# Performance work log

Measured on AMD Instinct MI355X. Metric: run time of the kernel, lower is better.

Reference implementation:

```python
import jax, jax.numpy as jnp
import numpy as np

N = 4096
IN_DIM = 512
NHEADS = 12
HEAD_DIM = 64


def setup_inputs() -> dict:
    key = jax.random.key(0)
    k_g, k_adj, k_wk, k_wq, k_hw = jax.random.split(key, 5)
    g = jax.random.normal(k_g, (N, IN_DIM), dtype=jnp.float32)
    # binary adjacency, broadcastable over the head axis of the [q,k,h] scores
    adj = jax.random.randint(k_adj, (N, N, 1), 0, 2).astype(jnp.float32)
    Wk = 0.002 * jax.random.normal(k_wk, (NHEADS, HEAD_DIM, IN_DIM), dtype=jnp.float32)
    Wq = 0.002 * jax.random.normal(k_wq, (NHEADS, HEAD_DIM, IN_DIM), dtype=jnp.float32)
    Hw = 0.002 * jax.random.normal(k_hw, (NHEADS, NHEADS), dtype=jnp.float32)
    Bk = jnp.zeros((NHEADS, HEAD_DIM), dtype=jnp.float32)
    Bq = jnp.zeros((NHEADS, HEAD_DIM), dtype=jnp.float32)
    betas = jnp.ones((NHEADS,), dtype=jnp.float32) / np.sqrt(HEAD_DIM).astype(np.float32)
    return {"g": g, "adj": adj, "Wk": Wk, "Wq": Wq, "Hw": Hw, "Bk": Bk, "Bq": Bq, "betas": betas}


def reference(g, adj, Wk, Wq, Hw, Bk, Bq, betas):
    def energy(g_):
        K = jnp.einsum('kd,hzd->khz', g_, Wk) + Bk          # [N, h, z]
        Q = jnp.einsum('qd,hzd->qhz', g_, Wq) + Bq          # [N, h, z]
        A1 = jnp.einsum('h,qhz,khz->hqk', betas, Q, K)      # [h, q, k]
        A11 = (jnp.transpose(A1, (1, 2, 0)) @ Hw) * adj      # [q, k, h], adjacency-gated
        A11 = jnp.where(A11 == 0, -jnp.inf, A11)
        A21 = jax.nn.logsumexp(A11, axis=1)                  # [q, h]
        A21 = jnp.where(A21 == -jnp.inf, 0.0, A21)
        A31 = A21.sum(0)                                     # [h]
        return ((-1.0 / betas) * A31).sum()
    # the module's __call__ returns (energy, dE/dg)
    return jax.value_and_grad(energy)(g)
```

## Files before the change

kernel.cpp:

```cpp
#include <hip/hip_runtime.h>
#include <stdint.h>

#define N_TOK 4096
#define DIM_IN 512
#define NH 12
#define HD 64
#define CDIM 768

using f32x4  = __attribute__((ext_vector_type(4))) float;
using f32x16 = __attribute__((ext_vector_type(16))) float;
using bf16x8 = __attribute__((ext_vector_type(8))) short;

static __device__ __forceinline__ unsigned short f2bf(float f){
    union { float f; unsigned int u; } v; v.f = f;
    unsigned int r = v.u + 0x7fffu + ((v.u >> 16) & 1u);
    return (unsigned short)(r >> 16);
}

__global__ __launch_bounds__(256) void proj_kernel(
    const float* __restrict__ g, const float* __restrict__ W,
    const float* __restrict__ B, const float* __restrict__ scale,
    unsigned short* __restrict__ out)
{
    __shared__ float at[16][68];
    __shared__ float bt[16][68];
    const int n0 = blockIdx.x * 64, c0 = blockIdx.y * 64;
    const int t  = threadIdx.x;
    const int tx = t & 15, ty = t >> 4;
    const int lr = t >> 2, lk = (t & 3) * 4;
    float acc[4][4] = {};
    f32x4 pg = *(const f32x4*)&g[(size_t)(n0 + lr) * DIM_IN + lk];
    f32x4 pw = *(const f32x4*)&W[(size_t)(c0 + lr) * DIM_IN + lk];
    for (int d0 = 0; d0 < DIM_IN; d0 += 16){
        __syncthreads();
        at[lk+0][lr] = pg[0]; at[lk+1][lr] = pg[1]; at[lk+2][lr] = pg[2]; at[lk+3][lr] = pg[3];
        bt[lk+0][lr] = pw[0]; bt[lk+1][lr] = pw[1]; bt[lk+2][lr] = pw[2]; bt[lk+3][lr] = pw[3];
        __syncthreads();
        {
            const int dn = (d0 + 16 < DIM_IN) ? d0 + 16 : 0;
            pg = *(const f32x4*)&g[(size_t)(n0 + lr) * DIM_IN + dn + lk];
            pw = *(const f32x4*)&W[(size_t)(c0 + lr) * DIM_IN + dn + lk];
        }
        #pragma unroll
        for (int kk = 0; kk < 16; kk++){
            f32x4 av = *(const f32x4*)&at[kk][ty*4];
            f32x4 bv = *(const f32x4*)&bt[kk][tx*4];
            #pragma unroll
            for (int i = 0; i < 4; i++)
                #pragma unroll
                for (int j = 0; j < 4; j++)
                    acc[i][j] += av[i] * bv[j];
        }
    }
    #pragma unroll
    for (int i = 0; i < 4; i++){
        const int n = n0 + ty*4 + i;
        #pragma unroll
        for (int j = 0; j < 4; j++){
            const int c = c0 + tx*4 + j;
            float v = acc[i][j] + B[c];
            if (scale) v *= scale[c >> 6];
            out[(size_t)n * CDIM + c] = f2bf(v);
        }
    }
}

#define TKF 32
#define KBS 776

__global__ __launch_bounds__(256, 2) void fwd_kernel(
    const unsigned short* __restrict__ Qb, const unsigned short* __restrict__ Kh,
    const float* __restrict__ adj, const float* __restrict__ HwG,
    float* __restrict__ l_ws, int seg_len)
{
    __shared__ unsigned short kbuf[TKF][KBS];
    __shared__ float hw[NH][12];
    const int t = threadIdx.x;
    if (t < NH * 12) hw[t / 12][t % 12] = HwG[t];
    const int lane = t & 63, wave = t >> 6;
    const int quad = lane >> 4, col = lane & 15;
    const int qt0 = blockIdx.x * 64 + wave * 16;
    const int kstart = blockIdx.y * seg_len;
    const unsigned short* qrow = &Qb[(size_t)(qt0 + col) * CDIM + quad*8];

    f32x4 l4[4][3];
    #pragma unroll
    for (int r = 0; r < 4; r++)
        #pragma unroll
        for (int j = 0; j < 3; j++)
            l4[r][j] = (f32x4){0.f,0.f,0.f,0.f};

    bf16x8 pk[12];
    #pragma unroll
    for (int i = 0; i < 12; i++){
        const int idx = t + 256 * i;
        const int row = idx / 96, cc = (idx % 96) * 8;
        pk[i] = *(const bf16x8*)&Kh[(size_t)(kstart + row) * CDIM + cc];
    }

    for (int kc = kstart; kc < kstart + seg_len; kc += TKF){
        __syncthreads();
        #pragma unroll
        for (int i = 0; i < 12; i++){
            const int idx = t + 256 * i;
            const int row = idx / 96, cc = (idx % 96) * 8;
            *(bf16x8*)&kbuf[row][cc] = pk[i];
        }
        __syncthreads();

        {
            const int nxt = kc + TKF;
            const int kcn = (nxt < kstart + seg_len) ? nxt : kstart;
            #pragma unroll
            for (int i = 0; i < 12; i++){
                const int idx = t + 256 * i;
                const int row = idx / 96, cc = (idx % 96) * 8;
                pk[i] = *(const bf16x8*)&Kh[(size_t)(kcn + row) * CDIM + cc];
            }
        }

        #pragma unroll
        for (int sub = 0; sub < 2; sub++){
            const int k0 = kc + sub * 16;
            float av[4];
            #pragma unroll
            for (int r = 0; r < 4; r++)
                av[r] = adj[(size_t)(qt0 + quad*4 + r) * N_TOK + k0 + col];

            const unsigned short* qp = qrow;
            asm volatile("" : "+v"(qp));

            f32x4 tv[4][3];
            #pragma unroll
            for (int r = 0; r < 4; r++)
                #pragma unroll
                for (int j = 0; j < 3; j++)
                    tv[r][j] = (f32x4){0.f,0.f,0.f,0.f};
            #pragma unroll
            for (int h = 0; h < NH; h++){
                bf16x8 a0 = *(const bf16x8*)&qp[h*HD];
                bf16x8 a1 = *(const bf16x8*)&qp[h*HD + 32];
                bf16x8 b0 = *(const bf16x8*)&kbuf[sub*16 + col][h*HD + quad*8];
                bf16x8 b1 = *(const bf16x8*)&kbuf[sub*16 + col][h*HD + 32 + quad*8];
                f32x4 s = {0.f,0.f,0.f,0.f};
                s = __builtin_amdgcn_mfma_f32_16x16x32_bf16(a0, b0, s, 0, 0, 0);
                s = __builtin_amdgcn_mfma_f32_16x16x32_bf16(a1, b1, s, 0, 0, 0);
                f32x4 w0 = *(const f32x4*)&hw[h][0];
                f32x4 w1 = *(const f32x4*)&hw[h][4];
                f32x4 w2 = *(const f32x4*)&hw[h][8];
                #pragma unroll
                for (int r = 0; r < 4; r++){
                    tv[r][0] += s[r] * w0;
                    tv[r][1] += s[r] * w1;
                    tv[r][2] += s[r] * w2;
                }
            }
            #pragma unroll
            for (int r = 0; r < 4; r++){
                #pragma unroll
                for (int j = 0; j < 3; j++){
                    #pragma unroll
                    for (int c = 0; c < 4; c++){
                        const float mm = tv[r][j][c] * av[r];
                        if (mm != 0.f) l4[r][j][c] += __expf(mm);
                    }
                }
            }
        }
    }
    #pragma unroll
    for (int r = 0; r < 4; r++)
        #pragma unroll
        for (int j = 0; j < 3; j++)
            #pragma unroll
            for (int c = 0; c < 4; c++){
                float v = l4[r][j][c];
                v += __shfl_xor(v, 1, 16);
                v += __shfl_xor(v, 2, 16);
                v += __shfl_xor(v, 4, 16);
                v += __shfl_xor(v, 8, 16);
                if (col == j*4 + c)
                    atomicAdd(&l_ws[(size_t)(qt0 + quad*4 + r) * NH + (j*4 + c)], v);
            }
}

__global__ __launch_bounds__(256) void lse_energy_kernel(
    const float* __restrict__ l_ws, float* __restrict__ lse_ws,
    const float* __restrict__ betas, float* __restrict__ energy)
{
    const int t = threadIdx.x;
    const int i = blockIdx.x * 256 + t;
    const float l = l_ws[i];
    float lse, ep;
    if (l > 0.f){ lse = logf(l); ep = -(1.f / betas[i % NH]) * lse; }
    else        { lse = -1e30f; ep = 0.f; }
    lse_ws[i] = lse;
    __shared__ float red[256];
    red[t] = ep;
    __syncthreads();
    for (int s = 128; s > 0; s >>= 1){
        if (t < s) red[t] += red[t + s];
        __syncthreads();
    }
    if (t == 0) atomicAdd(energy, red[0]);
}

#define CBS 776

template<int MODE>
__global__ __attribute__((amdgpu_flat_work_group_size(512, 512), amdgpu_waves_per_eu(2, 2)))
void bwd_kernel(
    const unsigned short* __restrict__ rowmat, const unsigned short* __restrict__ colmat,
    const float* __restrict__ adj, const float* __restrict__ HwG,
    const float* __restrict__ lse_ws, const float* __restrict__ betas,
    float* __restrict__ out_part, int seg_len)
{
    __shared__ unsigned short colbuf[64][CBS];
    __shared__ unsigned short dsbuf[NH][32][64];
    __shared__ float adjbuf[32][68];
    __shared__ float lsebuf[64 * NH];
    __shared__ float rowlse[32 * NH];
    __shared__ float invbuf[NH];
    __shared__ float hw[NH][12];
    const int t = threadIdx.x;
    if (t < NH * 12) hw[t / 12][t % 12] = HwG[t];
    if (t < NH) invbuf[t] = 1.f / betas[t];
    const int lane = t & 63, wave = t >> 6;
    const int quad = lane >> 4, col = lane & 15;
    const int rsub = wave >> 2, csub = wave & 3;
    const int n0 = csub * 16;
    const int rt0 = blockIdx.x * 32;
    const int rbase = rt0 + rsub * 16;
    const int cstart = blockIdx.y * seg_len;
    const int tA = n0 + col;

    if (MODE == 0 && t < 96)
        *(f32x4*)&rowlse[t*4] = *(const f32x4*)&lse_ws[(size_t)rt0 * NH + t*4];

    const unsigned short* rowp = &rowmat[(size_t)(rbase + col) * CDIM + quad*8];

    const int adj_m  = t >> 4, adj_nc = (t & 15) * 4;
    const int adj_qr = t >> 3, adj_kc = (t & 7) * 4;

    bf16x8 pcol[12];
    f32x4  padj;
    f32x4  plse = {0.f,0.f,0.f,0.f};
    {
        const int cb = cstart;
        #pragma unroll
        for (int i = 0; i < 12; i++){
            const int idx = t + 512 * i;
            const int row = idx / 96, cc = (idx % 96) * 8;
            pcol[i] = *(const bf16x8*)&colmat[(size_t)(cb + row) * CDIM + cc];
        }
        if (MODE == 0) padj = *(const f32x4*)&adj[(size_t)(rt0 + adj_m) * N_TOK + cb + adj_nc];
        else           padj = *(const f32x4*)&adj[(size_t)(cb + adj_qr) * N_TOK + rt0 + adj_kc];
        if (MODE == 1 && t < 192)
            plse = *(const f32x4*)&lse_ws[(size_t)cb * NH + t*4];
    }

    f32x16 accB32[3];
    #pragma unroll
    for (int gg = 0; gg < 3; gg++)
        #pragma unroll
        for (int q = 0; q < 16; q++) accB32[gg][q] = 0.f;

    for (int cb = cstart; cb < cstart + seg_len; cb += 64){
        __syncthreads();
        #pragma unroll
        for (int i = 0; i < 12; i++){
            const int idx = t + 512 * i;
            const int row = idx / 96, cc = (idx % 96) * 8;
            *(bf16x8*)&colbuf[row][cc ^ (((row >> 3) & 3) << 3)] = pcol[i];
        }
        if (MODE == 0){
            adjbuf[adj_m][adj_nc+0] = padj[0]; adjbuf[adj_m][adj_nc+1] = padj[1];
            adjbuf[adj_m][adj_nc+2] = padj[2]; adjbuf[adj_m][adj_nc+3] = padj[3];
        } else {
            adjbuf[adj_kc+0][adj_qr] = padj[0]; adjbuf[adj_kc+1][adj_qr] = padj[1];
            adjbuf[adj_kc+2][adj_qr] = padj[2]; adjbuf[adj_kc+3][adj_qr] = padj[3];
        }
        if (MODE == 1 && t < 192)
            *(f32x4*)&lsebuf[t*4] = plse;
        __syncthreads();

        const unsigned short* rp = rowp;
        asm volatile("" : "+v"(rp));

        {
            const int swzA = ((tA >> 3) & 3) << 3;
            f32x4 G[4][3];
            #pragma unroll
            for (int r = 0; r < 4; r++)
                #pragma unroll
                for (int j = 0; j < 3; j++)
                    G[r][j] = (f32x4){0.f,0.f,0.f,0.f};
            #pragma unroll
            for (int h = 0; h < NH; h++){
                bf16x8 a0 = *(const bf16x8*)&rp[h*HD];
                bf16x8 a1 = *(const bf16x8*)&rp[h*HD + 32];
                bf16x8 b0 = *(const bf16x8*)&colbuf[tA][(h*HD + quad*8) ^ swzA];
                bf16x8 b1 = *(const bf16x8*)&colbuf[tA][(h*HD + 32 + quad*8) ^ swzA];
                f32x4 s = {0.f,0.f,0.f,0.f};
                s = __builtin_amdgcn_mfma_f32_16x16x32_bf16(a0, b0, s, 0, 0, 0);
                s = __builtin_amdgcn_mfma_f32_16x16x32_bf16(a1, b1, s, 0, 0, 0);
                f32x4 w0 = *(const f32x4*)&hw[h][0];
                f32x4 w1 = *(const f32x4*)&hw[h][4];
                f32x4 w2 = *(const f32x4*)&hw[h][8];
                #pragma unroll
                for (int r = 0; r < 4; r++){
                    G[r][0] += s[r] * w0;
                    G[r][1] += s[r] * w1;
                    G[r][2] += s[r] * w2;
                }
            }
            #pragma unroll
            for (int r = 0; r < 4; r++){
                const float adjv = adjbuf[rsub*16 + quad*4 + r][tA];
                #pragma unroll
                for (int j = 0; j < 3; j++){
                    f32x4 lv;
                    if (MODE == 0) lv = *(const f32x4*)&rowlse[(rsub*16 + quad*4 + r) * NH + j*4];
                    else           lv = *(const f32x4*)&lsebuf[tA * NH + j*4];
                    #pragma unroll
                    for (int c = 0; c < 4; c++){
                        const float mm = G[r][j][c] * adjv;
                        const float p  = (mm != 0.f) ? __expf(mm - lv[c]) : 0.f;
                        G[r][j][c] = -invbuf[j*4 + c] * p;
                    }
                }
            }
            #pragma unroll
            for (int h = 0; h < NH; h++){
                f32x4 w0 = *(const f32x4*)&hw[h][0];
                f32x4 w1 = *(const f32x4*)&hw[h][4];
                f32x4 w2 = *(const f32x4*)&hw[h][8];
                #pragma unroll
                for (int r = 0; r < 4; r++){
                    f32x4 pr = G[r][0]*w0 + G[r][1]*w1 + G[r][2]*w2;
                    const float d = pr[0] + pr[1] + pr[2] + pr[3];
                    const int m = rsub*16 + quad*4 + r;
                    dsbuf[h][m][tA ^ ((m & 7) << 3)] = f2bf(d);
                }
            }
        }

        {
            const int nxt = cb + 64;
            const int cbn = (nxt < cstart + seg_len) ? nxt : cstart;
            #pragma unroll
            for (int i = 0; i < 12; i++){
                const int idx = t + 512 * i;
                const int row = idx / 96, cc = (idx % 96) * 8;
                pcol[i] = *(const bf16x8*)&colmat[(size_t)(cbn + row) * CDIM + cc];
            }
            if (MODE == 0) padj = *(const f32x4*)&adj[(size_t)(rt0 + adj_m) * N_TOK + cbn + adj_nc];
            else           padj = *(const f32x4*)&adj[(size_t)(cbn + adj_qr) * N_TOK + rt0 + adj_kc];
            if (MODE == 1 && t < 192)
                plse = *(const f32x4*)&lse_ws[(size_t)cbn * NH + t*4];
        }
        __syncthreads();

        {
            const int mB = lane & 31;
            const int halfB = lane >> 5;
            #pragma unroll
            for (int gg = 0; gg < 3; gg++){
                const int gidx = wave + gg*8;
                const int h = gidx >> 1, cg = gidx & 1;
                const int chL = h*HD + cg*32 + mB;
                f32x16 acc = accB32[gg];
                #pragma unroll
                for (int k0 = 0; k0 < 64; k0 += 16){
                    const int kbase = k0 + halfB*8;
                    bf16x8 a = *(const bf16x8*)&dsbuf[h][mB][kbase ^ ((mB & 7) << 3)];
                    const int sw = ((kbase >> 3) & 3) << 3;
                    const unsigned short* bp = &colbuf[kbase][chL ^ sw];
                    bf16x8 b;
                    #pragma unroll
                    for (int jj = 0; jj < 8; jj++)
                        b[jj] = (short)bp[jj * CBS];
                    acc = __builtin_amdgcn_mfma_f32_32x32x16_bf16(a, b, acc, 0, 0, 0);
                }
                accB32[gg] = acc;
            }
        }
    }
    float* outp = out_part + (size_t)blockIdx.y * N_TOK * CDIM;
    #pragma unroll
    for (int gg = 0; gg < 3; gg++){
        const int gidx = wave + gg*8;
        const int h = gidx >> 1, cg = gidx & 1;
        #pragma unroll
        for (int q = 0; q < 16; q++){
            const int i = (q & 3) + 8*(q >> 2) + 4*(lane >> 5);
            outp[(size_t)(rt0 + i) * CDIM + h*HD + cg*32 + (lane & 31)] = accB32[gg][q];
        }
    }
}

template<int NSEG>
__global__ __launch_bounds__(256) void final_dg_kernel(
    const float* __restrict__ dQbp, const float* __restrict__ dKhp,
    const float* __restrict__ Wq, const float* __restrict__ Wk,
    const float* __restrict__ betas, float* __restrict__ dg)
{
    __shared__ float at[16][68];
    __shared__ float bt[16][68];
    const int n0 = blockIdx.x * 64, d0 = blockIdx.y * 64;
    const int t  = threadIdx.x;
    const int tx = t & 15, ty = t >> 4;
    const int lr = t >> 2, lk = (t & 3) * 4;
    const int wk = t >> 4, wd = (t & 15) * 4;
    float acc[4][4] = {};

    f32x4 la[NSEG];
    f32x4 lw;
    auto issue = [&](int it){
        const int src = it / 48;
        const int c0i = (it % 48) * 16;
        const float* P = src ? dKhp : dQbp;
        const float* W = src ? Wk  : Wq;
        #pragma unroll
        for (int s = 0; s < NSEG; s++)
            la[s] = *(const f32x4*)&P[((size_t)s * N_TOK + n0 + lr) * CDIM + c0i + lk];
        lw = *(const f32x4*)&W[(size_t)(c0i + wk) * DIM_IN + d0 + wd];
    };
    issue(0);

    for (int it = 0; it < 96; it++){
        const int src = it / 48;
        const int c0i = (it % 48) * 16;
        __syncthreads();
        f32x4 a = la[0];
        #pragma unroll
        for (int s = 1; s < NSEG; s++) a += la[s];
        if (src == 0) a *= betas[(c0i + lk) >> 6];
        at[lk+0][lr] = a[0]; at[lk+1][lr] = a[1]; at[lk+2][lr] = a[2]; at[lk+3][lr] = a[3];
        bt[wk][wd+0] = lw[0]; bt[wk][wd+1] = lw[1]; bt[wk][wd+2] = lw[2]; bt[wk][wd+3] = lw[3];
        __syncthreads();
        issue(it + 1 < 96 ? it + 1 : 0);
        #pragma unroll
        for (int kk = 0; kk < 16; kk++){
            f32x4 av = *(const f32x4*)&at[kk][ty*4];
            f32x4 bv = *(const f32x4*)&bt[kk][tx*4];
            #pragma unroll
            for (int i = 0; i < 4; i++)
                #pragma unroll
                for (int j = 0; j < 4; j++)
                    acc[i][j] += av[i] * bv[j];
        }
    }
    #pragma unroll
    for (int i = 0; i < 4; i++)
        #pragma unroll
        for (int j = 0; j < 4; j++)
            dg[(size_t)(n0 + ty*4 + i) * DIM_IN + d0 + tx*4 + j] = acc[i][j];
}

extern "C" void kernel_launch(void* const* d_in, const int* in_sizes, int n_in,
                              void* d_out, int out_size, void* d_ws, size_t ws_size,
                              hipStream_t stream)
{
    const float* g     = (const float*)d_in[0];
    const float* adj   = (const float*)d_in[1];
    const float* Wk    = (const float*)d_in[2];
    const float* Wq    = (const float*)d_in[3];
    const float* Hw    = (const float*)d_in[4];
    const float* Bk    = (const float*)d_in[5];
    const float* Bq    = (const float*)d_in[6];
    const float* betas = (const float*)d_in[7];
    float* out = (float*)d_out;

    char* ws = (char*)d_ws;
    const size_t szQb   = (size_t)N_TOK * CDIM * sizeof(unsigned short);
    const size_t szL    = (size_t)N_TOK * NH * sizeof(float);
    const size_t szPart = (size_t)N_TOK * CDIM * sizeof(float);

    unsigned short* Qb = (unsigned short*)(ws);
    unsigned short* Kh = (unsigned short*)(ws + szQb);
    float* l_ws   = (float*)(ws + 2*szQb);
    float* lse_ws = (float*)(ws + 2*szQb + szL);
    char*  parts  = ws + 2*szQb + 2*szL;
    const size_t base = 2*szQb + 2*szL;

    int KS = 1;
    if      (ws_size >= base + 8*szPart) KS = 4;
    else if (ws_size >= base + 4*szPart) KS = 2;
    float* dQbp = (float*)parts;
    float* dKhp = (float*)(parts + (size_t)KS * szPart);

    hipMemsetAsync(l_ws, 0, szL, stream);
    hipMemsetAsync(d_out, 0, sizeof(float), stream);

    proj_kernel<<<dim3(64, 12), 256, 0, stream>>>(g, Wq, Bq, betas, Qb);
    proj_kernel<<<dim3(64, 12), 256, 0, stream>>>(g, Wk, Bk, nullptr, Kh);
    fwd_kernel<<<dim3(64, 8), 256, 0, stream>>>(Qb, Kh, adj, Hw, l_ws, N_TOK / 8);
    lse_energy_kernel<<<dim3(192), 256, 0, stream>>>(l_ws, lse_ws, betas, out);
    bwd_kernel<0><<<dim3(128, KS), 512, 0, stream>>>(Qb, Kh, adj, Hw, lse_ws, betas,
                                                     dQbp, N_TOK / KS);
    bwd_kernel<1><<<dim3(128, KS), 512, 0, stream>>>(Kh, Qb, adj, Hw, lse_ws, betas,
                                                     dKhp, N_TOK / KS);
    if (KS == 4)
        final_dg_kernel<4><<<dim3(64, 8), 256, 0, stream>>>(dQbp, dKhp, Wq, Wk, betas, out + 1);
    else if (KS == 2)
        final_dg_kernel<2><<<dim3(64, 8), 256, 0, stream>>>(dQbp, dKhp, Wq, Wk, betas, out + 1);
    else
        final_dg_kernel<1><<<dim3(64, 8), 256, 0, stream>>>(dQbp, dKhp, Wq, Wk, betas, out + 1);
}
```

Measured before the change: 1.388 ms.

## Load K tiles directly into LDS with swizzle, interleave chunks, merge projections

The forward kernel now loads each K chunk straight from global memory into LDS using global_load_lds, with an XOR swizzle replacing the padded row layout to avoid bank conflicts. This drops the register prefetch buffer, and blocks take 32-row chunks in a strided order over 12 y-blocks instead of 8 contiguous segments. Occupancy is raised to 3 blocks per CU. The two projection launches are merged into one grid with a z dimension. The cost is that the load-to-compute overlap from the old register prefetch is lost, since each chunk is now loaded and then waited on.

```diff
diff --git a/kernel.cpp b/kernel.cpp
--- a/kernel.cpp
+++ b/kernel.cpp
@@ -18,10 +18,18 @@
 }
 
 __global__ __launch_bounds__(256) void proj_kernel(
-    const float* __restrict__ g, const float* __restrict__ W,
-    const float* __restrict__ B, const float* __restrict__ scale,
-    unsigned short* __restrict__ out)
+    const float* __restrict__ g,
+    const float* __restrict__ Wq, const float* __restrict__ Wk,
+    const float* __restrict__ Bq, const float* __restrict__ Bk,
+    const float* __restrict__ betas,
+    unsigned short* __restrict__ Qb, unsigned short* __restrict__ Kh)
 {
+    const int z = blockIdx.z;
+    const float* W = z ? Wk : Wq;
+    const float* B = z ? Bk : Bq;
+    const float* scale = z ? nullptr : betas;
+    unsigned short* out = z ? Kh : Qb;
+
     __shared__ float at[16][68];
     __shared__ float bt[16][68];
     const int n0 = blockIdx.x * 64, c0 = blockIdx.y * 64;
@@ -65,23 +73,22 @@
     }
 }
 
-#define TKF 32
-#define KBS 776
-
-__global__ __launch_bounds__(256, 2) void fwd_kernel(
+#define NCH 128
+
+__global__ __launch_bounds__(256, 3) void fwd_kernel(
     const unsigned short* __restrict__ Qb, const unsigned short* __restrict__ Kh,
     const float* __restrict__ adj, const float* __restrict__ HwG,
-    float* __restrict__ l_ws, int seg_len)
+    float* __restrict__ l_ws)
 {
-    __shared__ unsigned short kbuf[TKF][KBS];
+    __shared__ unsigned short kbufF[32 * 768];
     __shared__ float hw[NH][12];
     const int t = threadIdx.x;
     if (t < NH * 12) hw[t / 12][t % 12] = HwG[t];
     const int lane = t & 63, wave = t >> 6;
     const int quad = lane >> 4, col = lane & 15;
     const int qt0 = blockIdx.x * 64 + wave * 16;
-    const int kstart = blockIdx.y * seg_len;
     const unsigned short* qrow = &Qb[(size_t)(qt0 + col) * CDIM + quad*8];
+    const int swr = (col & 7) << 3;
 
     f32x4 l4[4][3];
     #pragma unroll
@@ -90,34 +97,21 @@
         for (int j = 0; j < 3; j++)
             l4[r][j] = (f32x4){0.f,0.f,0.f,0.f};
 
-    bf16x8 pk[12];
-    #pragma unroll
-    for (int i = 0; i < 12; i++){
-        const int idx = t + 256 * i;
-        const int row = idx / 96, cc = (idx % 96) * 8;
-        pk[i] = *(const bf16x8*)&Kh[(size_t)(kstart + row) * CDIM + cc];
-    }
-
-    for (int kc = kstart; kc < kstart + seg_len; kc += TKF){
+    for (int ci = blockIdx.y; ci < NCH; ci += gridDim.y){
+        const int kc = ci * 32;
         __syncthreads();
         #pragma unroll
         for (int i = 0; i < 12; i++){
             const int idx = t + 256 * i;
             const int row = idx / 96, cc = (idx % 96) * 8;
-            *(bf16x8*)&kbuf[row][cc] = pk[i];
-        }
-        __syncthreads();
-
-        {
-            const int nxt = kc + TKF;
-            const int kcn = (nxt < kstart + seg_len) ? nxt : kstart;
-            #pragma unroll
-            for (int i = 0; i < 12; i++){
-                const int idx = t + 256 * i;
-                const int row = idx / 96, cc = (idx % 96) * 8;
-                pk[i] = *(const bf16x8*)&Kh[(size_t)(kcn + row) * CDIM + cc];
-            }
-        }
+            const unsigned short* src =
+                &Kh[(size_t)(kc + row) * CDIM + (cc ^ ((row & 7) << 3))];
+            __builtin_amdgcn_global_load_lds(
+                (const __attribute__((address_space(1))) unsigned int*)src,
+                (__attribute__((address_space(3))) unsigned int*)&kbufF[idx * 8],
+                16, 0, 0);
+        }
+        __syncthreads();
 
         #pragma unroll
         for (int sub = 0; sub < 2; sub++){
@@ -129,6 +123,7 @@
 
             const unsigned short* qp = qrow;
             asm volatile("" : "+v"(qp));
+            const unsigned short* kp = &kbufF[(sub*16 + col) * 768];
 
             f32x4 tv[4][3];
             #pragma unroll
@@ -140,8 +135,8 @@
             for (int h = 0; h < NH; h++){
                 bf16x8 a0 = *(const bf16x8*)&qp[h*HD];
                 bf16x8 a1 = *(const bf16x8*)&qp[h*HD + 32];
-                bf16x8 b0 = *(const bf16x8*)&kbuf[sub*16 + col][h*HD + quad*8];
-                bf16x8 b1 = *(const bf16x8*)&kbuf[sub*16 + col][h*HD + 32 + quad*8];
+                bf16x8 b0 = *(const bf16x8*)&kp[(h*HD + quad*8) ^ swr];
+                bf16x8 b1 = *(const bf16x8*)&kp[(h*HD + 32 + quad*8) ^ swr];
                 f32x4 s = {0.f,0.f,0.f,0.f};
                 s = __builtin_amdgcn_mfma_f32_16x16x32_bf16(a0, b0, s, 0, 0, 0);
                 s = __builtin_amdgcn_mfma_f32_16x16x32_bf16(a1, b1, s, 0, 0, 0);
@@ -493,9 +488,8 @@
     hipMemsetAsync(l_ws, 0, szL, stream);
     hipMemsetAsync(d_out, 0, sizeof(float), stream);
 
-    proj_kernel<<<dim3(64, 12), 256, 0, stream>>>(g, Wq, Bq, betas, Qb);
-    proj_kernel<<<dim3(64, 12), 256, 0, stream>>>(g, Wk, Bk, nullptr, Kh);
-    fwd_kernel<<<dim3(64, 8), 256, 0, stream>>>(Qb, Kh, adj, Hw, l_ws, N_TOK / 8);
+    proj_kernel<<<dim3(64, 12, 2), 256, 0, stream>>>(g, Wq, Wk, Bq, Bk, betas, Qb, Kh);
+    fwd_kernel<<<dim3(64, 12), 256, 0, stream>>>(Qb, Kh, adj, Hw, l_ws);
     lse_energy_kernel<<<dim3(192), 256, 0, stream>>>(l_ws, lse_ws, betas, out);
     bwd_kernel<0><<<dim3(128, KS), 512, 0, stream>>>(Qb, Kh, adj, Hw, lse_ws, betas,
                                                      dQbp, N_TOK / KS);
```

After: 1.544 ms. +11.2%, slower.
